# Kernel optimization log

Hardware: AMD Instinct MI355X
Metric: run time of the kernel (lower is better)

Reference implementation:

```python
import jax, jax.numpy as jnp
import numpy as np

N = 50000   # nodes
E = 800000  # edges
F = 128     # num_features
H = 128     # embedding_size
C = 10      # num_classes
G = 64      # graphs in batch


def setup_inputs() -> dict:
    key = jax.random.key(0)
    ks = jax.random.split(key, 12)
    x = jax.random.normal(ks[0], (N, F), dtype=jnp.float32)
    edge_index = jax.random.randint(ks[1], (2, E), 0, N, dtype=jnp.int32)
    batch_index = jnp.sort(jax.random.randint(ks[2], (N,), 0, G, dtype=jnp.int32))

    def lin(k, fan_in, fan_out):
        s = 1.0 / np.sqrt(fan_in)
        kw, kb = jax.random.split(k)
        W = jax.random.uniform(kw, (fan_in, fan_out), jnp.float32, -s, s)
        b = jax.random.uniform(kb, (fan_out,), jnp.float32, -s, s)
        return W, b

    W0, b0 = lin(ks[3], F, H)
    W1, b1 = lin(ks[4], H, H)
    W2, b2 = lin(ks[5], H, H)
    Wa, ba = lin(ks[6], 2 * H, C)
    return {"x": x, "edge_index": edge_index, "batch_index": batch_index,
            "W0": W0, "b0": b0, "W1": W1, "b1": b1, "W2": W2, "b2": b2,
            "Wa": Wa, "ba": ba}


def gcn_conv(x, src, dst, inv_sqrt_deg, W, b):
    # PyG GCNConv: h = x @ W; out_i = sum_{j->i} h_j / sqrt(d_j d_i)
    # with added self loops (deg already includes +1; self-loop term = h_i / d_i).
    h = x @ W                                             # [N, H]
    coef = inv_sqrt_deg[src] * inv_sqrt_deg[dst]          # [E]
    msg = coef[:, None] * h[src]                          # [E, H]
    agg = jax.ops.segment_sum(msg, dst, num_segments=N)   # [N, H]
    agg = agg + (inv_sqrt_deg * inv_sqrt_deg)[:, None] * h  # self loops
    return agg + b


def reference(x, edge_index, batch_index, W0, b0, W1, b1, W2, b2, Wa, ba):
    src, dst = edge_index[0], edge_index[1]
    # degree including self loop
    deg = jax.ops.segment_sum(jnp.ones((E,), x.dtype), dst, num_segments=N) + 1.0
    inv_sqrt_deg = jax.lax.rsqrt(deg)

    h = jax.nn.relu(gcn_conv(x, src, dst, inv_sqrt_deg, W0, b0))
    h = jax.nn.relu(gcn_conv(h, src, dst, inv_sqrt_deg, W1, b1))
    h = jax.nn.relu(gcn_conv(h, src, dst, inv_sqrt_deg, W2, b2))

    counts = jax.ops.segment_sum(jnp.ones((N,), x.dtype), batch_index, num_segments=G)
    sums = jax.ops.segment_sum(h, batch_index, num_segments=G)
    mean = sums / jnp.maximum(counts, 1.0)[:, None]
    mx = jax.ops.segment_max(h, batch_index, num_segments=G)
    mx = jnp.where(counts[:, None] > 0, mx, 0.0)

    aggr = jnp.concatenate([mean, mx], axis=1)            # [G, 2H]
    out = aggr @ Wa + ba                                  # [G, C]
    return out, aggr
```

## Files before the change

### kernel.cpp

```cpp
#include <hip/hip_runtime.h>
#include <stdint.h>

#define N_NODES 50000
#define N_EDGES 800000
#define HID 128
#define NCLS 10
#define NGRAPH 64
#define CAP 64

typedef unsigned short ushort_t;
typedef __attribute__((ext_vector_type(8))) short bf16x8;
typedef __attribute__((ext_vector_type(4))) float f32x4;
typedef __attribute__((ext_vector_type(4))) _Float16 f16x4;
typedef __attribute__((ext_vector_type(8))) _Float16 f16x8;

__device__ __forceinline__ ushort_t f2bf(float f) {
    union { float f; unsigned int i; } v; v.f = f;
    unsigned int u = v.i;
    return (ushort_t)((u + 0x7FFFu + ((u >> 16) & 1u)) >> 16);
}
__device__ __forceinline__ float bf2f(ushort_t u) {
    union { unsigned int i; float f; } v; v.i = ((unsigned int)u) << 16; return v.f;
}
__device__ __forceinline__ int exhi(int p) { return (p >> 16) & 0xffff; }
__device__ __forceinline__ int exlo(int p) { return p & 0xffff; }
__device__ __forceinline__ void add4h(float4& a, f16x4 v) {
    a.x += (float)v[0];
    a.y += (float)v[1];
    a.z += (float)v[2];
    a.w += (float)v[3];
}

__global__ void k_prep(const int* __restrict__ src, const int* __restrict__ dst,
                       int* cnt, ushort_t* csr16,
                       const int* __restrict__ batch, int* bound, int* counts,
                       const float* __restrict__ W0, const float* __restrict__ W1,
                       const float* __restrict__ W2, ushort_t* Whi, ushort_t* Wlo) {
    int b = blockIdx.x, t = threadIdx.x;
    if (b < 391) {
        int base = (b * 256 + t) * 8;
        if (base + 7 < N_EDGES) {
            int4 da = *(const int4*)(dst + base);
            int4 db = *(const int4*)(dst + base + 4);
            int4 sa = *(const int4*)(src + base);
            int4 sb = *(const int4*)(src + base + 4);
            int p0 = atomicAdd(&cnt[da.x], 1);
            int p1 = atomicAdd(&cnt[da.y], 1);
            int p2 = atomicAdd(&cnt[da.z], 1);
            int p3 = atomicAdd(&cnt[da.w], 1);
            int p4 = atomicAdd(&cnt[db.x], 1);
            int p5 = atomicAdd(&cnt[db.y], 1);
            int p6 = atomicAdd(&cnt[db.z], 1);
            int p7 = atomicAdd(&cnt[db.w], 1);
            if (p0 < CAP) csr16[da.x * CAP + p0] = (ushort_t)sa.x;
            if (p1 < CAP) csr16[da.y * CAP + p1] = (ushort_t)sa.y;
            if (p2 < CAP) csr16[da.z * CAP + p2] = (ushort_t)sa.z;
            if (p3 < CAP) csr16[da.w * CAP + p3] = (ushort_t)sa.w;
            if (p4 < CAP) csr16[db.x * CAP + p4] = (ushort_t)sb.x;
            if (p5 < CAP) csr16[db.y * CAP + p5] = (ushort_t)sb.y;
            if (p6 < CAP) csr16[db.z * CAP + p6] = (ushort_t)sb.z;
            if (p7 < CAP) csr16[db.w * CAP + p7] = (ushort_t)sb.w;
        } else {
            for (int i = base; i < N_EDGES; i++) {
                int d = dst[i];
                int slot = atomicAdd(&cnt[d], 1);
                if (slot < CAP) csr16[d * CAP + slot] = (ushort_t)src[i];
            }
        }
    } else if (b == 391) {
        int g = t;
        if (g <= NGRAPH) {
            int lo = 0, hi = N_NODES;
            while (lo < hi) {
                int mid = (lo + hi) >> 1;
                if (batch[mid] < g) lo = mid + 1; else hi = mid;
            }
            bound[g] = lo;
        }
        __syncthreads();
        if (g < NGRAPH) counts[g] = bound[g + 1] - bound[g];
    } else {
        int gid = (b - 392) * 256 + t;
        int l = gid / (32 * 512);
        int rem = gid - l * 32 * 512;
        int tile = rem >> 9;
        int p = rem & 511;
        int lane = p >> 3, j = p & 7;
        int kk = tile >> 3, c = tile & 7;
        int k = 32 * kk + (lane >> 4) * 8 + j;
        int n = 16 * c + (lane & 15);
        const float* W = (l == 0) ? W0 : (l == 1) ? W1 : W2;
        float x = W[k * 128 + n];
        ushort_t hi = f2bf(x);
        ushort_t lo = f2bf(x - bf2f(hi));
        Whi[l * 16384 + rem] = hi;
        Wlo[l * 16384 + rem] = lo;
    }
}

__global__ void k_cvt(const float* __restrict__ x, const int* __restrict__ cnt,
                      _Float16* __restrict__ X16) {
    int gid = blockIdx.x * 256 + threadIdx.x;
    int i = gid >> 4, seg = gid & 15;
    float isd = rsqrtf((float)cnt[i] + 1.0f);
    const f32x4* px = (const f32x4*)(x + (size_t)i * HID + seg * 8);
    f32x4 a = px[0], b = px[1];
    f16x8 o;
    o[0] = (_Float16)(isd * a.x); o[1] = (_Float16)(isd * a.y);
    o[2] = (_Float16)(isd * a.z); o[3] = (_Float16)(isd * a.w);
    o[4] = (_Float16)(isd * b.x); o[5] = (_Float16)(isd * b.y);
    o[6] = (_Float16)(isd * b.z); o[7] = (_Float16)(isd * b.w);
    *(f16x8*)(X16 + (size_t)i * HID + seg * 8) = o;
}

__global__ void k_layer(const _Float16* __restrict__ In,
                        const ushort_t* __restrict__ csr16, const int* __restrict__ cnt,
                        const ushort_t* __restrict__ Whi, const ushort_t* __restrict__ Wlo,
                        const float* __restrict__ bias, int scale_out,
                        int pool, const int* __restrict__ batch,
                        float* sums, float* maxs, _Float16* __restrict__ Out) {
    __shared__ float T[16][132];
    __shared__ int sg[16];
    int t = threadIdx.x, wv = t >> 6, lane = t & 63;
    int hl = lane & 31, q = lane >> 5;
    if (pool && t < 16) sg[t] = batch[blockIdx.x * 16 + t];

    for (int r = 0; r < 4; r++) {
        int i = blockIdx.x * 16 + wv * 4 + r;
        int ci = cnt[i];
        int m = min(ci, CAP);
        float isdi = rsqrtf((float)ci + 1.0f);
        int packed = ((const int*)(csr16 + (size_t)i * CAP))[hl];
        float4 a0 = make_float4(0.f, 0.f, 0.f, 0.f);
        float4 a1 = a0, a2 = a0, a3 = a0;
        if (q == 0) {
            f16x4 sv = *(const f16x4*)(In + (size_t)i * HID + hl * 4);
            add4h(a0, sv);
        }
        int e = 0;
        for (; e + 15 < m; e += 16) {
            int k0 = e >> 1;
            int p0 = __shfl(packed, k0);
            int p1 = __shfl(packed, k0 + 1);
            int p2 = __shfl(packed, k0 + 2);
            int p3 = __shfl(packed, k0 + 3);
            int p4 = __shfl(packed, k0 + 4);
            int p5 = __shfl(packed, k0 + 5);
            int p6 = __shfl(packed, k0 + 6);
            int p7 = __shfl(packed, k0 + 7);
            int s0 = q ? exhi(p0) : exlo(p0);
            int s1 = q ? exhi(p1) : exlo(p1);
            int s2 = q ? exhi(p2) : exlo(p2);
            int s3 = q ? exhi(p3) : exlo(p3);
            int s4 = q ? exhi(p4) : exlo(p4);
            int s5 = q ? exhi(p5) : exlo(p5);
            int s6 = q ? exhi(p6) : exlo(p6);
            int s7 = q ? exhi(p7) : exlo(p7);
            f16x4 v0 = *(const f16x4*)(In + (size_t)s0 * HID + hl * 4);
            f16x4 v1 = *(const f16x4*)(In + (size_t)s1 * HID + hl * 4);
            f16x4 v2 = *(const f16x4*)(In + (size_t)s2 * HID + hl * 4);
            f16x4 v3 = *(const f16x4*)(In + (size_t)s3 * HID + hl * 4);
            f16x4 v4 = *(const f16x4*)(In + (size_t)s4 * HID + hl * 4);
            f16x4 v5 = *(const f16x4*)(In + (size_t)s5 * HID + hl * 4);
            f16x4 v6 = *(const f16x4*)(In + (size_t)s6 * HID + hl * 4);
            f16x4 v7 = *(const f16x4*)(In + (size_t)s7 * HID + hl * 4);
            add4h(a0, v0); add4h(a1, v1); add4h(a2, v2); add4h(a3, v3);
            add4h(a0, v4); add4h(a1, v5); add4h(a2, v6); add4h(a3, v7);
        }
        for (; e + 7 < m; e += 8) {
            int k0 = e >> 1;
            int p0 = __shfl(packed, k0);
            int p1 = __shfl(packed, k0 + 1);
            int p2 = __shfl(packed, k0 + 2);
            int p3 = __shfl(packed, k0 + 3);
            int s0 = q ? exhi(p0) : exlo(p0);
            int s1 = q ? exhi(p1) : exlo(p1);
            int s2 = q ? exhi(p2) : exlo(p2);
            int s3 = q ? exhi(p3) : exlo(p3);
            f16x4 v0 = *(const f16x4*)(In + (size_t)s0 * HID + hl * 4);
            f16x4 v1 = *(const f16x4*)(In + (size_t)s1 * HID + hl * 4);
            f16x4 v2 = *(const f16x4*)(In + (size_t)s2 * HID + hl * 4);
            f16x4 v3 = *(const f16x4*)(In + (size_t)s3 * HID + hl * 4);
            add4h(a0, v0); add4h(a1, v1); add4h(a2, v2); add4h(a3, v3);
        }
        for (; e + 1 < m; e += 2) {
            int p = __shfl(packed, e >> 1);
            int s0 = q ? exhi(p) : exlo(p);
            f16x4 v0 = *(const f16x4*)(In + (size_t)s0 * HID + hl * 4);
            add4h(a0, v0);
        }
        if (e < m && q == 0) {
            int p = __shfl(packed, e >> 1);
            int s0 = exlo(p);
            f16x4 v0 = *(const f16x4*)(In + (size_t)s0 * HID + hl * 4);
            add4h(a0, v0);
        }
        float4 s4;
        s4.x = (a0.x + a1.x) + (a2.x + a3.x);
        s4.y = (a0.y + a1.y) + (a2.y + a3.y);
        s4.z = (a0.z + a1.z) + (a2.z + a3.z);
        s4.w = (a0.w + a1.w) + (a2.w + a3.w);
        s4.x += __shfl_xor(s4.x, 32);
        s4.y += __shfl_xor(s4.y, 32);
        s4.z += __shfl_xor(s4.z, 32);
        s4.w += __shfl_xor(s4.w, 32);
        if (q == 0) {
            float4 o;
            o.x = isdi * s4.x; o.y = isdi * s4.y;
            o.z = isdi * s4.z; o.w = isdi * s4.w;
            *(float4*)&T[wv * 4 + r][hl * 4] = o;
        }
    }
    __syncthreads();

    int mrow = lane & 15, qq = lane >> 4;
    f32x4 acc[2];
    acc[0] = (f32x4){0.f, 0.f, 0.f, 0.f};
    acc[1] = (f32x4){0.f, 0.f, 0.f, 0.f};
#pragma unroll
    for (int kk = 0; kk < 4; kk++) {
        const float* tp = &T[mrow][kk * 32 + qq * 8];
        float4 p0 = *(const float4*)tp;
        float4 p1 = *(const float4*)(tp + 4);
        float av[8] = {p0.x, p0.y, p0.z, p0.w, p1.x, p1.y, p1.z, p1.w};
        bf16x8 ahi, alo;
#pragma unroll
        for (int j = 0; j < 8; j++) {
            ushort_t hbits = f2bf(av[j]);
            ahi[j] = (short)hbits;
            alo[j] = (short)f2bf(av[j] - bf2f(hbits));
        }
#pragma unroll
        for (int cl = 0; cl < 2; cl++) {
            int c = wv * 2 + cl;
            const bf16x8 bhi = *(const bf16x8*)(Whi + (((kk * 8 + c) * 64 + lane) << 3));
            const bf16x8 blo = *(const bf16x8*)(Wlo + (((kk * 8 + c) * 64 + lane) << 3));
            acc[cl] = __builtin_amdgcn_mfma_f32_16x16x32_bf16(ahi, bhi, acc[cl], 0, 0, 0);
            acc[cl] = __builtin_amdgcn_mfma_f32_16x16x32_bf16(alo, bhi, acc[cl], 0, 0, 0);
            acc[cl] = __builtin_amdgcn_mfma_f32_16x16x32_bf16(ahi, blo, acc[cl], 0, 0, 0);
        }
    }
    int rb = blockIdx.x * 16 + qq * 4;
    if (!pool) {
        float osc[4];
#pragma unroll
        for (int rr = 0; rr < 4; rr++)
            osc[rr] = scale_out ? rsqrtf((float)cnt[rb + rr] + 1.0f) : 1.0f;
#pragma unroll
        for (int cl = 0; cl < 2; cl++) {
            int col = (wv * 2 + cl) * 16 + mrow;
            float bcol = bias[col];
#pragma unroll
            for (int rr = 0; rr < 4; rr++) {
                float val = fmaxf(acc[cl][rr] + bcol, 0.f);
                Out[(size_t)(rb + rr) * HID + col] = (_Float16)(val * osc[rr]);
            }
        }
    } else {
        __syncthreads();
#pragma unroll
        for (int cl = 0; cl < 2; cl++) {
            int col = (wv * 2 + cl) * 16 + mrow;
            float bcol = bias[col];
#pragma unroll
            for (int rr = 0; rr < 4; rr++)
                T[qq * 4 + rr][col] = fmaxf(acc[cl][rr] + bcol, 0.f);
        }
        __syncthreads();
        int f = t & 127, half = t >> 7;
        int cur = sg[0];
        float s = 0.f, mx = 0.f;
        for (int r = 0; r < 16; r++) {
            int g = sg[r];
            if (g != cur) {
                if (half == 0) atomicAdd(&sums[cur * HID + f], s);
                else atomicMax((int*)&maxs[cur * HID + f], __float_as_int(mx));
                s = 0.f; mx = 0.f; cur = g;
            }
            float v = T[r][f];
            s += v;
            mx = fmaxf(mx, v);
        }
        if (half == 0) atomicAdd(&sums[cur * HID + f], s);
        else atomicMax((int*)&maxs[cur * HID + f], __float_as_int(mx));
    }
}

__global__ void k_final(const float* __restrict__ sums, const float* __restrict__ maxs,
                        const int* __restrict__ counts, const float* __restrict__ Wa,
                        const float* __restrict__ ba, float* __restrict__ out) {
    __shared__ float a[256];
    __shared__ float red[4];
    int g = blockIdx.x, t = threadIdx.x;
    float denom = fmaxf((float)counts[g], 1.f);
    float val = (t < 128) ? (sums[g * HID + t] / denom) : maxs[g * HID + (t - 128)];
    a[t] = val;
    out[NGRAPH * NCLS + g * 256 + t] = val;
    __syncthreads();
    for (int c = 0; c < NCLS; c++) {
        float p = a[t] * Wa[t * NCLS + c];
        for (int o = 32; o > 0; o >>= 1) p += __shfl_down(p, o);
        if ((t & 63) == 0) red[t >> 6] = p;
        __syncthreads();
        if (t == 0) {
            out[g * NCLS + c] = red[0] + red[1] + red[2] + red[3] + ba[c];
        }
        __syncthreads();
    }
}

extern "C" void kernel_launch(void* const* d_in, const int* in_sizes, int n_in,
                              void* d_out, int out_size, void* d_ws, size_t ws_size,
                              hipStream_t stream) {
    const float* x = (const float*)d_in[0];
    const int* ei = (const int*)d_in[1];
    const int* src = ei;
    const int* dst = ei + N_EDGES;
    const int* batch = (const int*)d_in[2];
    const float* W0 = (const float*)d_in[3];
    const float* b0 = (const float*)d_in[4];
    const float* W1 = (const float*)d_in[5];
    const float* b1 = (const float*)d_in[6];
    const float* W2 = (const float*)d_in[7];
    const float* b2 = (const float*)d_in[8];
    const float* Wa = (const float*)d_in[9];
    const float* ba = (const float*)d_in[10];
    float* out = (float*)d_out;

    char* ws = (char*)d_ws;
    int*       cnt    = (int*)(ws + 0);
    int*       bound  = (int*)(ws + 200192);
    int*       counts = (int*)(ws + 200576);
    float*     sums   = (float*)(ws + 200832);
    float*     maxs   = (float*)(ws + 233600);
    ushort_t*  Whi    = (ushort_t*)(ws + 266368);
    ushort_t*  Wlo    = (ushort_t*)(ws + 364672);
    ushort_t*  csr16  = (ushort_t*)(ws + 462976);
    _Float16*  X16    = (_Float16*)(ws + 7462976);
    _Float16*  hA     = (_Float16*)(ws + 20262976);
    _Float16*  hB     = (_Float16*)(ws + 33062976);

    hipMemsetAsync(ws, 0, 266368, stream);
    k_prep<<<584, 256, 0, stream>>>(src, dst, cnt, csr16, batch, bound, counts,
                                    W0, W1, W2, Whi, Wlo);
    k_cvt<<<3125, 256, 0, stream>>>(x, cnt, X16);

    k_layer<<<3125, 256, 0, stream>>>(X16, csr16, cnt, Whi, Wlo, b0, 1,
                                      0, batch, sums, maxs, hA);
    k_layer<<<3125, 256, 0, stream>>>(hA, csr16, cnt, Whi + 16384, Wlo + 16384, b1, 1,
                                      0, batch, sums, maxs, hB);
    k_layer<<<3125, 256, 0, stream>>>(hB, csr16, cnt, Whi + 32768, Wlo + 32768, b2, 0,
                                      1, batch, sums, maxs, hA);

    k_final<<<NGRAPH, 256, 0, stream>>>(sums, maxs, counts, Wa, ba, out);
}
```

Baseline: 270.2 us.

## Fuse x conversion into prep and final readout into last layer

The separate k_cvt kernel is folded into k_prep as extra blocks that convert x to fp16 without the degree scaling. Layer 0 instead applies the per-source inverse sqrt degree inside the gather loop by reading cnt for each neighbour. The k_final kernel is removed: the last 64 blocks of the final layer, chosen by an atomic ticket counter, spin until all tiles have finished and then compute the pooled readout and classifier. This saves two kernel launches and a pass over x, at the cost of extra cnt loads in layer 0, a narrower unroll there, and a spin-wait that depends on all blocks making progress.

```diff
diff --git a/kernel.cpp b/kernel.cpp
--- a/kernel.cpp
+++ b/kernel.cpp
@@ -7,6 +7,7 @@
 #define NCLS 10
 #define NGRAPH 64
 #define CAP 64
+#define NTILES 3125
 
 typedef unsigned short ushort_t;
 typedef __attribute__((ext_vector_type(8))) short bf16x8;
@@ -30,12 +31,19 @@
     a.z += (float)v[2];
     a.w += (float)v[3];
 }
+__device__ __forceinline__ void fmad4h(float4& a, float d, f16x4 v) {
+    a.x = fmaf(d, (float)v[0], a.x);
+    a.y = fmaf(d, (float)v[1], a.y);
+    a.z = fmaf(d, (float)v[2], a.z);
+    a.w = fmaf(d, (float)v[3], a.w);
+}
 
 __global__ void k_prep(const int* __restrict__ src, const int* __restrict__ dst,
                        int* cnt, ushort_t* csr16,
                        const int* __restrict__ batch, int* bound, int* counts,
                        const float* __restrict__ W0, const float* __restrict__ W1,
-                       const float* __restrict__ W2, ushort_t* Whi, ushort_t* Wlo) {
+                       const float* __restrict__ W2, ushort_t* Whi, ushort_t* Wlo,
+                       const float* __restrict__ x, _Float16* __restrict__ X16) {
     int b = blockIdx.x, t = threadIdx.x;
     if (b < 391) {
         int base = (b * 256 + t) * 8;
@@ -79,7 +87,7 @@
         }
         __syncthreads();
         if (g < NGRAPH) counts[g] = bound[g + 1] - bound[g];
-    } else {
+    } else if (b < 584) {
         int gid = (b - 392) * 256 + t;
         int l = gid / (32 * 512);
         int rem = gid - l * 32 * 512;
@@ -90,37 +98,37 @@
         int k = 32 * kk + (lane >> 4) * 8 + j;
         int n = 16 * c + (lane & 15);
         const float* W = (l == 0) ? W0 : (l == 1) ? W1 : W2;
-        float x = W[k * 128 + n];
-        ushort_t hi = f2bf(x);
-        ushort_t lo = f2bf(x - bf2f(hi));
+        float xv = W[k * 128 + n];
+        ushort_t hi = f2bf(xv);
+        ushort_t lo = f2bf(xv - bf2f(hi));
         Whi[l * 16384 + rem] = hi;
         Wlo[l * 16384 + rem] = lo;
+    } else {
+        int gid = (b - 584) * 256 + t;
+        int i = gid >> 4, seg = gid & 15;
+        const f32x4* px = (const f32x4*)(x + (size_t)i * HID + seg * 8);
+        f32x4 a = px[0], bb = px[1];
+        f16x8 o;
+        o[0] = (_Float16)a.x;  o[1] = (_Float16)a.y;
+        o[2] = (_Float16)a.z;  o[3] = (_Float16)a.w;
+        o[4] = (_Float16)bb.x; o[5] = (_Float16)bb.y;
+        o[6] = (_Float16)bb.z; o[7] = (_Float16)bb.w;
+        *(f16x8*)(X16 + (size_t)i * HID + seg * 8) = o;
     }
-}
-
-__global__ void k_cvt(const float* __restrict__ x, const int* __restrict__ cnt,
-                      _Float16* __restrict__ X16) {
-    int gid = blockIdx.x * 256 + threadIdx.x;
-    int i = gid >> 4, seg = gid & 15;
-    float isd = rsqrtf((float)cnt[i] + 1.0f);
-    const f32x4* px = (const f32x4*)(x + (size_t)i * HID + seg * 8);
-    f32x4 a = px[0], b = px[1];
-    f16x8 o;
-    o[0] = (_Float16)(isd * a.x); o[1] = (_Float16)(isd * a.y);
-    o[2] = (_Float16)(isd * a.z); o[3] = (_Float16)(isd * a.w);
-    o[4] = (_Float16)(isd * b.x); o[5] = (_Float16)(isd * b.y);
-    o[6] = (_Float16)(isd * b.z); o[7] = (_Float16)(isd * b.w);
-    *(f16x8*)(X16 + (size_t)i * HID + seg * 8) = o;
 }
 
 __global__ void k_layer(const _Float16* __restrict__ In,
                         const ushort_t* __restrict__ csr16, const int* __restrict__ cnt,
                         const ushort_t* __restrict__ Whi, const ushort_t* __restrict__ Wlo,
-                        const float* __restrict__ bias, int scale_out,
+                        const float* __restrict__ bias, int pre_scaled, int scale_out,
                         int pool, const int* __restrict__ batch,
-                        float* sums, float* maxs, _Float16* __restrict__ Out) {
+                        float* sums, float* maxs, _Float16* __restrict__ Out,
+                        int* done, const int* __restrict__ counts,
+                        const float* __restrict__ Wa, const float* __restrict__ ba,
+                        float* __restrict__ out) {
     __shared__ float T[16][132];
     __shared__ int sg[16];
+    __shared__ int sord;
     int t = threadIdx.x, wv = t >> 6, lane = t & 63;
     int hl = lane & 31, q = lane >> 5;
     if (pool && t < 16) sg[t] = batch[blockIdx.x * 16 + t];
@@ -135,65 +143,104 @@
         float4 a1 = a0, a2 = a0, a3 = a0;
         if (q == 0) {
             f16x4 sv = *(const f16x4*)(In + (size_t)i * HID + hl * 4);
-            add4h(a0, sv);
+            float sfac = pre_scaled ? 1.0f : isdi;
+            fmad4h(a0, sfac, sv);
         }
         int e = 0;
-        for (; e + 15 < m; e += 16) {
-            int k0 = e >> 1;
-            int p0 = __shfl(packed, k0);
-            int p1 = __shfl(packed, k0 + 1);
-            int p2 = __shfl(packed, k0 + 2);
-            int p3 = __shfl(packed, k0 + 3);
-            int p4 = __shfl(packed, k0 + 4);
-            int p5 = __shfl(packed, k0 + 5);
-            int p6 = __shfl(packed, k0 + 6);
-            int p7 = __shfl(packed, k0 + 7);
-            int s0 = q ? exhi(p0) : exlo(p0);
-            int s1 = q ? exhi(p1) : exlo(p1);
-            int s2 = q ? exhi(p2) : exlo(p2);
-            int s3 = q ? exhi(p3) : exlo(p3);
-            int s4 = q ? exhi(p4) : exlo(p4);
-            int s5 = q ? exhi(p5) : exlo(p5);
-            int s6 = q ? exhi(p6) : exlo(p6);
-            int s7 = q ? exhi(p7) : exlo(p7);
-            f16x4 v0 = *(const f16x4*)(In + (size_t)s0 * HID + hl * 4);
-            f16x4 v1 = *(const f16x4*)(In + (size_t)s1 * HID + hl * 4);
-            f16x4 v2 = *(const f16x4*)(In + (size_t)s2 * HID + hl * 4);
-            f16x4 v3 = *(const f16x4*)(In + (size_t)s3 * HID + hl * 4);
-            f16x4 v4 = *(const f16x4*)(In + (size_t)s4 * HID + hl * 4);
-            f16x4 v5 = *(const f16x4*)(In + (size_t)s5 * HID + hl * 4);
-            f16x4 v6 = *(const f16x4*)(In + (size_t)s6 * HID + hl * 4);
-            f16x4 v7 = *(const f16x4*)(In + (size_t)s7 * HID + hl * 4);
-            add4h(a0, v0); add4h(a1, v1); add4h(a2, v2); add4h(a3, v3);
-            add4h(a0, v4); add4h(a1, v5); add4h(a2, v6); add4h(a3, v7);
-        }
-        for (; e + 7 < m; e += 8) {
-            int k0 = e >> 1;
-            int p0 = __shfl(packed, k0);
-            int p1 = __shfl(packed, k0 + 1);
-            int p2 = __shfl(packed, k0 + 2);
-            int p3 = __shfl(packed, k0 + 3);
-            int s0 = q ? exhi(p0) : exlo(p0);
-            int s1 = q ? exhi(p1) : exlo(p1);
-            int s2 = q ? exhi(p2) : exlo(p2);
-            int s3 = q ? exhi(p3) : exlo(p3);
-            f16x4 v0 = *(const f16x4*)(In + (size_t)s0 * HID + hl * 4);
-            f16x4 v1 = *(const f16x4*)(In + (size_t)s1 * HID + hl * 4);
-            f16x4 v2 = *(const f16x4*)(In + (size_t)s2 * HID + hl * 4);
-            f16x4 v3 = *(const f16x4*)(In + (size_t)s3 * HID + hl * 4);
-            add4h(a0, v0); add4h(a1, v1); add4h(a2, v2); add4h(a3, v3);
-        }
-        for (; e + 1 < m; e += 2) {
-            int p = __shfl(packed, e >> 1);
-            int s0 = q ? exhi(p) : exlo(p);
-            f16x4 v0 = *(const f16x4*)(In + (size_t)s0 * HID + hl * 4);
-            add4h(a0, v0);
-        }
-        if (e < m && q == 0) {
-            int p = __shfl(packed, e >> 1);
-            int s0 = exlo(p);
-            f16x4 v0 = *(const f16x4*)(In + (size_t)s0 * HID + hl * 4);
-            add4h(a0, v0);
+        if (pre_scaled) {
+            for (; e + 15 < m; e += 16) {
+                int k0 = e >> 1;
+                int p0 = __shfl(packed, k0);
+                int p1 = __shfl(packed, k0 + 1);
+                int p2 = __shfl(packed, k0 + 2);
+                int p3 = __shfl(packed, k0 + 3);
+                int p4 = __shfl(packed, k0 + 4);
+                int p5 = __shfl(packed, k0 + 5);
+                int p6 = __shfl(packed, k0 + 6);
+                int p7 = __shfl(packed, k0 + 7);
+                int s0 = q ? exhi(p0) : exlo(p0);
+                int s1 = q ? exhi(p1) : exlo(p1);
+                int s2 = q ? exhi(p2) : exlo(p2);
+                int s3 = q ? exhi(p3) : exlo(p3);
+                int s4 = q ? exhi(p4) : exlo(p4);
+                int s5 = q ? exhi(p5) : exlo(p5);
+                int s6 = q ? exhi(p6) : exlo(p6);
+                int s7 = q ? exhi(p7) : exlo(p7);
+                f16x4 v0 = *(const f16x4*)(In + (size_t)s0 * HID + hl * 4);
+                f16x4 v1 = *(const f16x4*)(In + (size_t)s1 * HID + hl * 4);
+                f16x4 v2 = *(const f16x4*)(In + (size_t)s2 * HID + hl * 4);
+                f16x4 v3 = *(const f16x4*)(In + (size_t)s3 * HID + hl * 4);
+                f16x4 v4 = *(const f16x4*)(In + (size_t)s4 * HID + hl * 4);
+                f16x4 v5 = *(const f16x4*)(In + (size_t)s5 * HID + hl * 4);
+                f16x4 v6 = *(const f16x4*)(In + (size_t)s6 * HID + hl * 4);
+                f16x4 v7 = *(const f16x4*)(In + (size_t)s7 * HID + hl * 4);
+                add4h(a0, v0); add4h(a1, v1); add4h(a2, v2); add4h(a3, v3);
+                add4h(a0, v4); add4h(a1, v5); add4h(a2, v6); add4h(a3, v7);
+            }
+            for (; e + 7 < m; e += 8) {
+                int k0 = e >> 1;
+                int p0 = __shfl(packed, k0);
+                int p1 = __shfl(packed, k0 + 1);
+                int p2 = __shfl(packed, k0 + 2);
+                int p3 = __shfl(packed, k0 + 3);
+                int s0 = q ? exhi(p0) : exlo(p0);
+                int s1 = q ? exhi(p1) : exlo(p1);
+                int s2 = q ? exhi(p2) : exlo(p2);
+                int s3 = q ? exhi(p3) : exlo(p3);
+                f16x4 v0 = *(const f16x4*)(In + (size_t)s0 * HID + hl * 4);
+                f16x4 v1 = *(const f16x4*)(In + (size_t)s1 * HID + hl * 4);
+                f16x4 v2 = *(const f16x4*)(In + (size_t)s2 * HID + hl * 4);
+                f16x4 v3 = *(const f16x4*)(In + (size_t)s3 * HID + hl * 4);
+                add4h(a0, v0); add4h(a1, v1); add4h(a2, v2); add4h(a3, v3);
+            }
+            for (; e + 1 < m; e += 2) {
+                int p = __shfl(packed, e >> 1);
+                int s0 = q ? exhi(p) : exlo(p);
+                f16x4 v0 = *(const f16x4*)(In + (size_t)s0 * HID + hl * 4);
+                add4h(a0, v0);
+            }
+            if (e < m && q == 0) {
+                int p = __shfl(packed, e >> 1);
+                int s0 = exlo(p);
+                f16x4 v0 = *(const f16x4*)(In + (size_t)s0 * HID + hl * 4);
+                add4h(a0, v0);
+            }
+        } else {
+            for (; e + 7 < m; e += 8) {
+                int k0 = e >> 1;
+                int p0 = __shfl(packed, k0);
+                int p1 = __shfl(packed, k0 + 1);
+                int p2 = __shfl(packed, k0 + 2);
+                int p3 = __shfl(packed, k0 + 3);
+                int s0 = q ? exhi(p0) : exlo(p0);
+                int s1 = q ? exhi(p1) : exlo(p1);
+                int s2 = q ? exhi(p2) : exlo(p2);
+                int s3 = q ? exhi(p3) : exlo(p3);
+                float d0 = rsqrtf((float)cnt[s0] + 1.0f);
+                float d1 = rsqrtf((float)cnt[s1] + 1.0f);
+                float d2 = rsqrtf((float)cnt[s2] + 1.0f);
+                float d3 = rsqrtf((float)cnt[s3] + 1.0f);
+                f16x4 v0 = *(const f16x4*)(In + (size_t)s0 * HID + hl * 4);
+                f16x4 v1 = *(const f16x4*)(In + (size_t)s1 * HID + hl * 4);
+                f16x4 v2 = *(const f16x4*)(In + (size_t)s2 * HID + hl * 4);
+                f16x4 v3 = *(const f16x4*)(In + (size_t)s3 * HID + hl * 4);
+                fmad4h(a0, d0, v0); fmad4h(a1, d1, v1);
+                fmad4h(a2, d2, v2); fmad4h(a3, d3, v3);
+            }
+            for (; e + 1 < m; e += 2) {
+                int p = __shfl(packed, e >> 1);
+                int s0 = q ? exhi(p) : exlo(p);
+                float d0 = rsqrtf((float)cnt[s0] + 1.0f);
+                f16x4 v0 = *(const f16x4*)(In + (size_t)s0 * HID + hl * 4);
+                fmad4h(a0, d0, v0);
+            }
+            if (e < m && q == 0) {
+                int p = __shfl(packed, e >> 1);
+                int s0 = exlo(p);
+                float d0 = rsqrtf((float)cnt[s0] + 1.0f);
+                f16x4 v0 = *(const f16x4*)(In + (size_t)s0 * HID + hl * 4);
+                fmad4h(a0, d0, v0);
+            }
         }
         float4 s4;
         s4.x = (a0.x + a1.x) + (a2.x + a3.x);
@@ -283,29 +330,34 @@
         }
         if (half == 0) atomicAdd(&sums[cur * HID + f], s);
         else atomicMax((int*)&maxs[cur * HID + f], __float_as_int(mx));
-    }
-}
-
-__global__ void k_final(const float* __restrict__ sums, const float* __restrict__ maxs,
-                        const int* __restrict__ counts, const float* __restrict__ Wa,
-                        const float* __restrict__ ba, float* __restrict__ out) {
-    __shared__ float a[256];
-    __shared__ float red[4];
-    int g = blockIdx.x, t = threadIdx.x;
-    float denom = fmaxf((float)counts[g], 1.f);
-    float val = (t < 128) ? (sums[g * HID + t] / denom) : maxs[g * HID + (t - 128)];
-    a[t] = val;
-    out[NGRAPH * NCLS + g * 256 + t] = val;
-    __syncthreads();
-    for (int c = 0; c < NCLS; c++) {
-        float p = a[t] * Wa[t * NCLS + c];
-        for (int o = 32; o > 0; o >>= 1) p += __shfl_down(p, o);
-        if ((t & 63) == 0) red[t >> 6] = p;
+
+        __threadfence();
         __syncthreads();
-        if (t == 0) {
-            out[g * NCLS + c] = red[0] + red[1] + red[2] + red[3] + ba[c];
-        }
+        if (t == 0) sord = atomicAdd(done, 1);
         __syncthreads();
+        int ord = sord;
+        if (ord >= NTILES - NGRAPH) {
+            int g = ord - (NTILES - NGRAPH);
+            if (t == 0) { while (atomicAdd(done, 0) < NTILES) {} }
+            __syncthreads();
+            float* a = &T[0][0];
+            float denom = fmaxf((float)counts[g], 1.f);
+            float val;
+            if (t < 128) val = atomicAdd(&sums[g * HID + t], 0.0f) / denom;
+            else val = __int_as_float(atomicMax((int*)&maxs[g * HID + (t - 128)], 0));
+            a[t] = val;
+            out[NGRAPH * NCLS + g * 256 + t] = val;
+            __syncthreads();
+            for (int c = 0; c < NCLS; c++) {
+                float p = a[t] * Wa[t * NCLS + c];
+                for (int o = 32; o > 0; o >>= 1) p += __shfl_down(p, o);
+                if ((t & 63) == 0) a[256 + (t >> 6)] = p;
+                __syncthreads();
+                if (t == 0)
+                    out[g * NCLS + c] = a[256] + a[257] + a[258] + a[259] + ba[c];
+                __syncthreads();
+            }
+        }
     }
 }
 
@@ -330,6 +382,7 @@
     char* ws = (char*)d_ws;
     int*       cnt    = (int*)(ws + 0);
     int*       bound  = (int*)(ws + 200192);
+    int*       done   = (int*)(ws + 200512);
     int*       counts = (int*)(ws + 200576);
     float*     sums   = (float*)(ws + 200832);
     float*     maxs   = (float*)(ws + 233600);
@@ -341,16 +394,16 @@
     _Float16*  hB     = (_Float16*)(ws + 33062976);
 
     hipMemsetAsync(ws, 0, 266368, stream);
-    k_prep<<<584, 256, 0, stream>>>(src, dst, cnt, csr16, batch, bound, counts,
-                                    W0, W1, W2, Whi, Wlo);
-    k_cvt<<<3125, 256, 0, stream>>>(x, cnt, X16);
-
-    k_layer<<<3125, 256, 0, stream>>>(X16, csr16, cnt, Whi, Wlo, b0, 1,
-                                      0, batch, sums, maxs, hA);
-    k_layer<<<3125, 256, 0, stream>>>(hA, csr16, cnt, Whi + 16384, Wlo + 16384, b1, 1,
-                                      0, batch, sums, maxs, hB);
-    k_layer<<<3125, 256, 0, stream>>>(hB, csr16, cnt, Whi + 32768, Wlo + 32768, b2, 0,
-                                      1, batch, sums, maxs, hA);
-
-    k_final<<<NGRAPH, 256, 0, stream>>>(sums, maxs, counts, Wa, ba, out);
-}
+    k_prep<<<3709, 256, 0, stream>>>(src, dst, cnt, csr16, batch, bound, counts,
+                                     W0, W1, W2, Whi, Wlo, x, X16);
+
+    k_layer<<<NTILES, 256, 0, stream>>>(X16, csr16, cnt, Whi, Wlo, b0, 0, 1,
+                                        0, batch, sums, maxs, hA,
+                                        done, counts, Wa, ba, out);
+    k_layer<<<NTILES, 256, 0, stream>>>(hA, csr16, cnt, Whi + 16384, Wlo + 16384, b1, 1, 1,
+                                        0, batch, sums, maxs, hB,
+                                        done, counts, Wa, ba, out);
+    k_layer<<<NTILES, 256, 0, stream>>>(hB, csr16, cnt, Whi + 32768, Wlo + 32768, b2, 1, 0,
+                                        1, batch, sums, maxs, hA,
+                                        done, counts, Wa, ba, out);
+}
```

After: 514.2 us. 90.3% more time.
